# Kernel tuning notes

Measured on AMD Instinct MI355X. Metric: run time of the kernel, lower is better.

The kernel has to match this reference:

```python
import jax, jax.numpy as jnp
import numpy as np

B, N, E, H, D = 8, 1024, 512, 8, 64  # batch, tokens, embed, heads, dim_head


def setup_inputs() -> dict:
    key = jax.random.key(0)
    ks = jax.random.split(key, 12)
    f = lambda k, s: jax.random.normal(k, s, dtype=jnp.float32)
    return {
        "x": f(ks[0], (B, N, E)),
        "r_t": f(ks[1], (B, N, E)),
        "r_c": f(ks[2], (B, N, E)),
        "bias_time_e": f(ks[3], (H, D)) * 0.02,
        "bias_time_r": f(ks[4], (H, D)) * 0.02,
        "bias_channel_r": f(ks[5], (H, D)) * 0.02,
        "bias_channel_e": f(ks[6], (H, D)) * 0.02,
        "w_qkv": f(ks[7], (E, 3 * H * D)) * 0.02,   # to_qkv (no bias)
        "w_kr_t": f(ks[8], (E, H * D)) * 0.02,      # k_r_time_net (no bias)
        "w_kr_c": f(ks[9], (E, H * D)) * 0.02,      # k_r_channel_net (no bias)
        "w_out": f(ks[10], (H * D, E)) * 0.02,      # to_out Linear
        "b_out": f(ks[11], (E,)) * 0.02,
    }


def _rel_shift(x):
    # x: [i, j, b, h] -- TransformerXL relative shift along j
    i, j, b, h = x.shape
    zp = jnp.zeros((i, 1, b, h), x.dtype)
    xp = jnp.concatenate([zp, x], axis=1).reshape(j + 1, i, b, h)
    return xp[1:].reshape(i, j, b, h)


def reference(x, r_t, r_c, bias_time_e, bias_time_r, bias_channel_r, bias_channel_e,
              w_qkv, w_kr_t, w_kr_c, w_out, b_out):
    b, n, _ = x.shape
    to_nbhd = lambda t: t.reshape(b, n, H, D).transpose(1, 0, 2, 3)  # [n,b,h,d]
    q, k, v = jnp.split(x @ w_qkv, 3, axis=-1)
    q, k, v = to_nbhd(q), to_nbhd(k), to_nbhd(v)
    qb = q + bias_time_e  # broadcast [h,d] over [n,b,h,d]
    wr_t = to_nbhd(r_t @ w_kr_t)
    wr_c = to_nbhd(r_c @ w_kr_c)
    AC = jnp.einsum('ibhd,jbhd->ijbh', qb, k)
    BD_t = _rel_shift(jnp.einsum('ibhd,jbhd->ijbh', qb, wr_t))
    BD_c = _rel_shift(jnp.einsum('ibhd,jbhd->ijbh', qb, wr_c))
    dots = AC + (BD_t + BD_c) * 0.5
    # Faithful to torch: nn.Softmax(dim=-1) on [i,j,b,h] normalizes over HEADS.
    attn = jax.nn.softmax(dots, axis=-1)
    out = jnp.einsum('ijbh,jbhd->ibhd', attn, v)
    out = out.transpose(1, 0, 2, 3).reshape(b, n, H * D) @ w_out + b_out
    return out, attn.transpose(2, 3, 0, 1)  # ([b,n,E], [b,h,q,k])
```

## Files before the change

### kernel.cpp

```cpp
#include <hip/hip_runtime.h>
#include <hip/hip_fp16.h>


typedef _Float16 f16;
typedef f16 f16x4 __attribute__((ext_vector_type(4)));
typedef f16 f16x8 __attribute__((ext_vector_type(8)));
typedef float f32x4 __attribute__((ext_vector_type(4)));

#define MFMA16(a,b,c) __builtin_amdgcn_mfma_f32_16x16x32_f16((a),(b),(c),0,0,0)

static __device__ __forceinline__ size_t qpidx(int bh, int q, int d) {
  return ((((size_t)bh * 64 + (q >> 4)) * 2 + (d >> 5)) * 64 +
          ((q & 15) + (((d >> 3) & 3) << 4))) * 8 + (d & 7);
}
static __device__ __forceinline__ size_t vpidx(int bh, int d, int j) {
  return ((((size_t)bh * 4 + (d >> 4)) * 32 + (j >> 5)) * 64 +
          ((d & 15) + (((j >> 3) & 3) << 4))) * 8 + (j & 7);
}

__global__ __launch_bounds__(256) void kprep(
    const float* __restrict__ x, const float* __restrict__ rt, const float* __restrict__ rc,
    const float* __restrict__ wqkv, const float* __restrict__ wkrt, const float* __restrict__ wkrc,
    f16* __restrict__ X16, f16* __restrict__ A2, f16* __restrict__ WQ, f16* __restrict__ W2)
{
  const int t = threadIdx.x, gx = blockIdx.x, mode = blockIdx.y;
  if (mode <= 2) {
    const size_t id = (size_t)gx * 256 + t;
    const float* src = (mode == 0) ? x : (mode == 1) ? rt : rc;
    float4 v0 = *(const float4*)&src[id * 8];
    float4 v1 = *(const float4*)&src[id * 8 + 4];
    f16x8 o = {(f16)v0.x, (f16)v0.y, (f16)v0.z, (f16)v0.w,
               (f16)v1.x, (f16)v1.y, (f16)v1.z, (f16)v1.w};
    if (mode == 0) *(f16x8*)&X16[id * 8] = o;
    else {
      const int mrow = (int)(id >> 6), cc = (int)(id & 63);
      *(f16x8*)&A2[(size_t)mrow * 1024 + (mode == 2 ? 512 : 0) + cc * 8] = o;
    }
  } else if (mode == 3) {
    if (gx >= 384) return;
    const int c = gx & 63, n = (gx >> 6) * 256 + t;
    f16x8 o;
    #pragma unroll
    for (int e = 0; e < 8; ++e) o[e] = (f16)wqkv[(size_t)(c * 8 + e) * 1536 + n];
    *(f16x8*)&WQ[(size_t)n * 512 + c * 8] = o;
  } else {
    if (gx >= 128) return;
    const int c = gx & 63, n = (gx >> 6) * 256 + t;
    const float* src = (mode == 4) ? wkrt : wkrc;
    f16x8 o;
    #pragma unroll
    for (int e = 0; e < 8; ++e) o[e] = (f16)src[(size_t)(c * 8 + e) * 512 + n];
    *(f16x8*)&W2[(size_t)n * 1024 + (mode == 5 ? 512 : 0) + c * 8] = o;
  }
}

__global__ __launch_bounds__(256) void kproj(
    const f16* __restrict__ X16, const f16* __restrict__ A2,
    const f16* __restrict__ WQ, const f16* __restrict__ W2,
    const float* __restrict__ bias_te,
    f16* __restrict__ QP, f16* __restrict__ KP, f16* __restrict__ VP, f16* __restrict__ WP)
{
  __shared__ f16 As[128 * 64];
  __shared__ f16 Bs[128 * 64];
  const int t = threadIdx.x, l = t & 63, w = t >> 6;
  const int wr = w >> 1, wc = w & 1;
  const int m0 = blockIdx.x * 128;
  const int y = blockIdx.y;
  const int mode = y >> 2;
  const bool wrs = (mode == 3);
  const f16* Asrc = wrs ? A2 : X16;
  const int lda = wrs ? 1024 : 512;
  const int K = wrs ? 1024 : 512;
  const f16* Bsrc = wrs ? (W2 + (size_t)((y - 12) * 128) * 1024)
                        : (WQ + (size_t)(y * 128) * 512);
  const int ldb = wrs ? 1024 : 512;

  f32x4 acc[4][4] = {};
  for (int k0 = 0; k0 < K; k0 += 64) {
    __syncthreads();
    #pragma unroll
    for (int rep = 0; rep < 4; ++rep) {
      const int idx = rep * 256 + t;
      const int row = idx >> 3, kb = idx & 7;
      const int slot = (kb ^ (row & 7)) << 3;
      f16x8 va = *(const f16x8*)&Asrc[(size_t)(m0 + row) * lda + k0 + kb * 8];
      *(f16x8*)&As[row * 64 + slot] = va;
      f16x8 vb = *(const f16x8*)&Bsrc[(size_t)row * ldb + k0 + kb * 8];
      *(f16x8*)&Bs[row * 64 + slot] = vb;
    }
    __syncthreads();
    #pragma unroll
    for (int kc = 0; kc < 2; ++kc) {
      f16x8 af[4], bf[4];
      const int kb = kc * 4 + (l >> 4);
      #pragma unroll
      for (int mb = 0; mb < 4; ++mb) {
        const int r = wr * 64 + mb * 16 + (l & 15);
        af[mb] = *(const f16x8*)&As[r * 64 + ((kb ^ (r & 7)) << 3)];
      }
      #pragma unroll
      for (int nb = 0; nb < 4; ++nb) {
        const int r = wc * 64 + nb * 16 + (l & 15);
        bf[nb] = *(const f16x8*)&Bs[r * 64 + ((kb ^ (r & 7)) << 3)];
      }
      #pragma unroll
      for (int mb = 0; mb < 4; ++mb)
      #pragma unroll
      for (int nb = 0; nb < 4; ++nb)
        acc[mb][nb] = MFMA16(af[mb], bf[nb], acc[mb][nb]);
    }
  }
  #pragma unroll
  for (int mb = 0; mb < 4; ++mb)
  #pragma unroll
  for (int nb = 0; nb < 4; ++nb) {
    const int loc = wc * 64 + nb * 16 + (l & 15);
    const int c = (y & 3) * 128 + loc;
    const int hh = c >> 6, d = c & 63;
    const float badd = (mode == 0) ? bias_te[c] : 0.f;
    f32x4 a = acc[mb][nb];
    #pragma unroll
    for (int r = 0; r < 4; ++r) {
      const int m = m0 + wr * 64 + mb * 16 + (l >> 4) * 4 + r;
      const int bb = m >> 10, tn = m & 1023;
      const int bh = bb * 8 + hh;
      const float v = a[r] + badd;
      if (mode == 0)      QP[qpidx(bh, tn, d)] = (f16)v;
      else if (mode == 1) KP[qpidx(bh, tn, d)] = (f16)v;
      else if (mode == 2) VP[vpidx(bh, d, tn)] = (f16)v;
      else                WP[qpidx(bh, tn, d)] = (f16)v;
    }
  }
}

__global__ __launch_bounds__(512) void kdots(
    const f16* __restrict__ QP, const f16* __restrict__ KP,
    const f16* __restrict__ WP, float* __restrict__ attn_out)
{
  __shared__ f16 sd[8][32][72];
  const int t = threadIdx.x, l = t & 63, h = t >> 6;
  const int k0 = blockIdx.x * 64;
  const int q0 = blockIdx.y * 32;
  const int b = blockIdx.z;
  const int bh = b * 8 + h;
  const f16x8* QP8 = (const f16x8*)QP;
  const f16x8* KP8 = (const f16x8*)KP;
  const f16x8* WP8 = (const f16x8*)WP;
  f16x8 aq[3][2];
  #pragma unroll
  for (int mb = 0; mb < 3; ++mb)
  #pragma unroll
  for (int kc = 0; kc < 2; ++kc)
    aq[mb][kc] = QP8[((size_t)(bh * 64 + (q0 >> 4) + mb) * 2 + kc) * 64 + l];
  {
    f16* sdf = (f16*)sd;
    for (int i = t; i < 2304; i += 512) *(f16x8*)&sdf[(size_t)i * 8] = f16x8{};
  }
  __syncthreads();
  const int u0 = k0 - q0;
  const int qrow = (l >> 4) * 4;
  auto rawblock = [&](int jb) {
    f32x4 racc[3] = {};
    #pragma unroll
    for (int kc = 0; kc < 2; ++kc) {
      f16x8 bf = WP8[((size_t)(bh * 64 + jb) * 2 + kc) * 64 + l];
      #pragma unroll
      for (int mb = 0; mb < 3; ++mb)
        racc[mb] = MFMA16(aq[mb][kc], bf, racc[mb]);
    }
    const int jglob = jb * 16 + (l & 15);
    #pragma unroll
    for (int mb = 0; mb < 3; ++mb)
    #pragma unroll
    for (int r = 0; r < 4; ++r) {
      const int qloc = mb * 16 + qrow + r;
      const int a = q0 + qloc;
      const f16 v = (f16)(0.5f * racc[mb][r]);
      if (qloc < 32) {
        const int kA = a + jglob - 1023;
        if (kA >= k0 && kA < k0 + 64) sd[h][qloc][kA - k0] = v;
      }
      if (qloc >= 1 && qloc <= 32) {
        const int kB = a + jglob + 1;
        if (kB >= k0 && kB < k0 + 64) sd[h][qloc - 1][kB - k0] = v;
      }
    }
  };
  {
    const int blo_e = u0 - 33, bhi_e = (u0 + 61 > 1023) ? 1023 : u0 + 61;
    if (bhi_e >= 0) {
      const int blo = (blo_e < 0 ? 0 : blo_e) >> 4, bhi = bhi_e >> 4;
      for (int jb = blo; jb <= bhi; ++jb) rawblock(jb);
    }
    if (u0 <= 31) {
      const int alo_e = 992 + u0, ahi_e = (1086 + u0 > 1023) ? 1023 : 1086 + u0;
      const int alo = (alo_e < 0 ? 0 : alo_e) >> 4, ahi = ahi_e >> 4;
      for (int jb = alo; jb <= ahi; ++jb) rawblock(jb);
    }
  }
  __syncthreads();
  f32x4 acc[2][4] = {};
  #pragma unroll
  for (int kc = 0; kc < 2; ++kc) {
    #pragma unroll
    for (int nb = 0; nb < 4; ++nb) {
      f16x8 bf = KP8[((size_t)(bh * 64 + (k0 >> 4) + nb) * 2 + kc) * 64 + l];
      #pragma unroll
      for (int mb = 0; mb < 2; ++mb)
        acc[mb][nb] = MFMA16(aq[mb][kc], bf, acc[mb][nb]);
    }
  }
  #pragma unroll
  for (int mb = 0; mb < 2; ++mb)
  #pragma unroll
  for (int nb = 0; nb < 4; ++nb)
  #pragma unroll
  for (int r = 0; r < 4; ++r) {
    const int qloc = mb * 16 + qrow + r, kloc = nb * 16 + (l & 15);
    sd[h][qloc][kloc] = (f16)((float)sd[h][qloc][kloc] + acc[mb][nb][r]);
  }
  __syncthreads();
  {
    const int o = t * 4, q = o >> 6, k = o & 63;
    float dv[8][4];
    #pragma unroll
    for (int hh = 0; hh < 8; ++hh) {
      f16x4 v = *(const f16x4*)&sd[hh][q][k];
      dv[hh][0] = (float)v[0]; dv[hh][1] = (float)v[1];
      dv[hh][2] = (float)v[2]; dv[hh][3] = (float)v[3];
    }
    #pragma unroll
    for (int e = 0; e < 4; ++e) {
      float m = dv[0][e];
      #pragma unroll
      for (int hh = 1; hh < 8; ++hh) m = fmaxf(m, dv[hh][e]);
      float ssum = 0.f;
      #pragma unroll
      for (int hh = 0; hh < 8; ++hh) { float a = __expf(dv[hh][e] - m); dv[hh][e] = a; ssum += a; }
      float rinv = 1.f / ssum;
      #pragma unroll
      for (int hh = 0; hh < 8; ++hh) dv[hh][e] *= rinv;
    }
    const size_t qg = q0 + q;
    #pragma unroll
    for (int hh = 0; hh < 8; ++hh)
      *(float4*)&attn_out[((size_t)(b * 8 + hh) * 1024 + qg) * 1024 + k0 + k] =
          float4{dv[hh][0], dv[hh][1], dv[hh][2], dv[hh][3]};
  }
}

__global__ __launch_bounds__(256) void kpv(
    const float* __restrict__ attn, const f16* __restrict__ VP, f16* __restrict__ OUT1)
{
  __shared__ f16 at[128][72];
  const int t = threadIdx.x, l = t & 63, w = t >> 6;
  const int q0 = blockIdx.x * 128;
  const int bh = blockIdx.y;
  const int b = bh >> 3, h = bh & 7;
  const size_t abase = (size_t)bh * 1024 * 1024;
  const f16x8* VP8 = (const f16x8*)VP;
  f32x4 acc[2][4] = {};
  for (int j0 = 0; j0 < 1024; j0 += 64) {
    __syncthreads();
    #pragma unroll
    for (int rep = 0; rep < 8; ++rep) {
      int idx = rep * 1024 + t * 4;
      int q = idx >> 6, j = idx & 63;
      float4 v = *(const float4*)&attn[abase + (size_t)(q0 + q) * 1024 + j0 + j];
      *(f16x4*)&at[q][j] = f16x4{(f16)v.x, (f16)v.y, (f16)v.z, (f16)v.w};
    }
    __syncthreads();
    #pragma unroll
    for (int kc = 0; kc < 2; ++kc) {
      f16x8 pa[2];
      #pragma unroll
      for (int mb = 0; mb < 2; ++mb) {
        int row = w * 32 + mb * 16 + (l & 15);
        int jj = kc * 32 + (l >> 4) * 8;
        pa[mb] = *(const f16x8*)&at[row][jj];
      }
      #pragma unroll
      for (int nb = 0; nb < 4; ++nb) {
        f16x8 vb = VP8[(((size_t)bh * 4 + nb) * 32 + (j0 >> 5) + kc) * 64 + l];
        #pragma unroll
        for (int mb = 0; mb < 2; ++mb)
          acc[mb][nb] = MFMA16(pa[mb], vb, acc[mb][nb]);
      }
    }
  }
  #pragma unroll
  for (int mb = 0; mb < 2; ++mb)
  #pragma unroll
  for (int nb = 0; nb < 4; ++nb)
  #pragma unroll
  for (int r = 0; r < 4; ++r) {
    const int qg = q0 + w * 32 + mb * 16 + (l >> 4) * 4 + r;
    const int dd = nb * 16 + (l & 15);
    OUT1[((size_t)b * 1024 + qg) * 512 + h * 64 + dd] = (f16)acc[mb][nb][r];
  }
}

__global__ __launch_bounds__(256) void kout(
    const f16* __restrict__ OUT1, const float* __restrict__ w_out,
    const float* __restrict__ b_out, float* __restrict__ out)
{
  __shared__ f16 a_s[128][36];
  __shared__ f16 b_s[64][36];
  const int t = threadIdx.x, l = t & 63, w = t >> 6;
  const int m0 = blockIdx.x * 128;
  const int c0 = blockIdx.y * 64;
  f32x4 acc[2][4] = {};
  for (int k0 = 0; k0 < 512; k0 += 32) {
    __syncthreads();
    #pragma unroll
    for (int rep = 0; rep < 2; ++rep) {
      int idx = rep * 2048 + t * 8;
      int r = idx >> 5, c = idx & 31;
      f16x8 v = *(const f16x8*)&OUT1[(size_t)(m0 + r) * 512 + k0 + c];
      *(f16x4*)&a_s[r][c]     = f16x4{v[0], v[1], v[2], v[3]};
      *(f16x4*)&a_s[r][c + 4] = f16x4{v[4], v[5], v[6], v[7]};
    }
    #pragma unroll
    for (int rep = 0; rep < 2; ++rep) {
      int idx = rep * 1024 + t * 4;
      int kr = idx >> 6, c = idx & 63;
      float4 v = *(const float4*)&w_out[(size_t)(k0 + kr) * 512 + c0 + c];
      b_s[c + 0][kr] = (f16)v.x; b_s[c + 1][kr] = (f16)v.y;
      b_s[c + 2][kr] = (f16)v.z; b_s[c + 3][kr] = (f16)v.w;
    }
    __syncthreads();
    const int kc = (l >> 4) * 8;
    f16x8 af[2];
    #pragma unroll
    for (int mb = 0; mb < 2; ++mb) {
      int r = w * 32 + mb * 16 + (l & 15);
      af[mb] = __builtin_shufflevector(*(const f16x4*)&a_s[r][kc], *(const f16x4*)&a_s[r][kc + 4],
                                       0, 1, 2, 3, 4, 5, 6, 7);
    }
    #pragma unroll
    for (int nb = 0; nb < 4; ++nb) {
      int cc = nb * 16 + (l & 15);
      f16x8 bf = __builtin_shufflevector(*(const f16x4*)&b_s[cc][kc], *(const f16x4*)&b_s[cc][kc + 4],
                                         0, 1, 2, 3, 4, 5, 6, 7);
      #pragma unroll
      for (int mb = 0; mb < 2; ++mb)
        acc[mb][nb] = MFMA16(af[mb], bf, acc[mb][nb]);
    }
  }
  #pragma unroll
  for (int mb = 0; mb < 2; ++mb)
  #pragma unroll
  for (int nb = 0; nb < 4; ++nb) {
    const int cg = c0 + nb * 16 + (l & 15);
    const float bb = b_out[cg];
    #pragma unroll
    for (int r = 0; r < 4; ++r) {
      const int m = m0 + w * 32 + mb * 16 + (l >> 4) * 4 + r;
      out[(size_t)m * 512 + cg] = acc[mb][nb][r] + bb;
    }
  }
}

extern "C" void kernel_launch(void* const* d_in, const int* in_sizes, int n_in,
                              void* d_out, int out_size, void* d_ws, size_t ws_size,
                              hipStream_t stream) {
  const float* x       = (const float*)d_in[0];
  const float* rt      = (const float*)d_in[1];
  const float* rc      = (const float*)d_in[2];
  const float* bias_te = (const float*)d_in[3];
  const float* w_qkv   = (const float*)d_in[7];
  const float* w_kr_t  = (const float*)d_in[8];
  const float* w_kr_c  = (const float*)d_in[9];
  const float* w_out   = (const float*)d_in[10];
  const float* b_out   = (const float*)d_in[11];
  float* out = (float*)d_out;
  float* attn_out = out + (size_t)8 * 1024 * 512;

  const size_t oX16 = 0;
  const size_t oA2  = oX16 + 4194304;
  const size_t oWQ  = oA2  + 8388608;
  const size_t oW2  = oWQ  + 786432;
  const size_t oQP  = oW2  + 524288;
  const size_t oKP  = oQP  + 4194304;
  const size_t oVP  = oKP  + 4194304;
  const size_t oWP  = oVP  + 4194304;
  const size_t oO1  = oWP  + 4194304;
  const size_t NEEDED = (oO1 + 4194304) * 2;
  if (ws_size < NEEDED) return;
  f16* ws = (f16*)d_ws;
  f16 *X16 = ws + oX16, *A2 = ws + oA2, *WQ = ws + oWQ, *W2 = ws + oW2;
  f16 *QP = ws + oQP, *KP = ws + oKP, *VP = ws + oVP, *WP = ws + oWP;
  f16 *OUT1 = ws + oO1;

  kprep<<<dim3(2048, 6), 256, 0, stream>>>(x, rt, rc, w_qkv, w_kr_t, w_kr_c,
                                           X16, A2, WQ, W2);
  kproj<<<dim3(64, 16), 256, 0, stream>>>(X16, A2, WQ, W2, bias_te, QP, KP, VP, WP);
  kdots<<<dim3(16, 32, 8), 512, 0, stream>>>(QP, KP, WP, attn_out);
  kpv<<<dim3(8, 64), 256, 0, stream>>>(attn_out, VP, OUT1);
  kout<<<dim3(64, 8), 256, 0, stream>>>(OUT1, w_out, b_out, out);
}
```

Before: 257.1 us.

## Fuse attention-times-V into dots kernel with split-K partial outputs

The separate kpv kernel, which re-read the full fp32 attention matrix from global memory, is removed. kdots now loops over four key tiles per block, keeps the softmaxed probabilities in shared memory as f16 and multiplies them by V directly, accumulating into registers. Each of the four key groups writes an fp32 partial output, and kout sums the four partials while loading its A operand. This avoids re-reading the large attention tensor, at the cost of extra fp32 partial-output traffic, a 4x smaller kdots grid and added syncs per tile.

```diff
diff --git a/kernel.cpp b/kernel.cpp
--- a/kernel.cpp
+++ b/kernel.cpp
@@ -133,141 +133,130 @@
   }
 }
 
-__global__ __launch_bounds__(512) void kdots(
+__global__ __launch_bounds__(512, 4) void kdots(
     const f16* __restrict__ QP, const f16* __restrict__ KP,
-    const f16* __restrict__ WP, float* __restrict__ attn_out)
+    const f16* __restrict__ WP, const f16* __restrict__ VP,
+    float* __restrict__ attn_out, float* __restrict__ OUTP)
 {
   __shared__ f16 sd[8][32][72];
   const int t = threadIdx.x, l = t & 63, h = t >> 6;
-  const int k0 = blockIdx.x * 64;
+  const int kg = blockIdx.x;
   const int q0 = blockIdx.y * 32;
   const int b = blockIdx.z;
   const int bh = b * 8 + h;
   const f16x8* QP8 = (const f16x8*)QP;
   const f16x8* KP8 = (const f16x8*)KP;
   const f16x8* WP8 = (const f16x8*)WP;
+  const f16x8* VP8 = (const f16x8*)VP;
+  const int qrow = (l >> 4) * 4;
   f16x8 aq[3][2];
   #pragma unroll
   for (int mb = 0; mb < 3; ++mb)
   #pragma unroll
   for (int kc = 0; kc < 2; ++kc)
     aq[mb][kc] = QP8[((size_t)(bh * 64 + (q0 >> 4) + mb) * 2 + kc) * 64 + l];
-  {
-    f16* sdf = (f16*)sd;
-    for (int i = t; i < 2304; i += 512) *(f16x8*)&sdf[(size_t)i * 8] = f16x8{};
-  }
-  __syncthreads();
-  const int u0 = k0 - q0;
-  const int qrow = (l >> 4) * 4;
-  auto rawblock = [&](int jb) {
-    f32x4 racc[3] = {};
-    #pragma unroll
-    for (int kc = 0; kc < 2; ++kc) {
-      f16x8 bf = WP8[((size_t)(bh * 64 + jb) * 2 + kc) * 64 + l];
+
+  f32x4 oacc[2][4] = {};
+
+  for (int kti = 0; kti < 4; ++kti) {
+    const int k0 = (kg * 4 + kti) * 64;
+    {
+      f16* sdf = (f16*)sd;
+      for (int i = t; i < 2304; i += 512) *(f16x8*)&sdf[(size_t)i * 8] = f16x8{};
+    }
+    __syncthreads();
+    const int u0 = k0 - q0;
+    auto rawblock = [&](int jb) {
+      f32x4 racc[3] = {};
+      #pragma unroll
+      for (int kc = 0; kc < 2; ++kc) {
+        f16x8 bf = WP8[((size_t)(bh * 64 + jb) * 2 + kc) * 64 + l];
+        #pragma unroll
+        for (int mb = 0; mb < 3; ++mb)
+          racc[mb] = MFMA16(aq[mb][kc], bf, racc[mb]);
+      }
+      const int jglob = jb * 16 + (l & 15);
       #pragma unroll
       for (int mb = 0; mb < 3; ++mb)
-        racc[mb] = MFMA16(aq[mb][kc], bf, racc[mb]);
-    }
-    const int jglob = jb * 16 + (l & 15);
-    #pragma unroll
-    for (int mb = 0; mb < 3; ++mb)
-    #pragma unroll
-    for (int r = 0; r < 4; ++r) {
-      const int qloc = mb * 16 + qrow + r;
-      const int a = q0 + qloc;
-      const f16 v = (f16)(0.5f * racc[mb][r]);
-      if (qloc < 32) {
-        const int kA = a + jglob - 1023;
-        if (kA >= k0 && kA < k0 + 64) sd[h][qloc][kA - k0] = v;
-      }
-      if (qloc >= 1 && qloc <= 32) {
-        const int kB = a + jglob + 1;
-        if (kB >= k0 && kB < k0 + 64) sd[h][qloc - 1][kB - k0] = v;
-      }
-    }
-  };
-  {
-    const int blo_e = u0 - 33, bhi_e = (u0 + 61 > 1023) ? 1023 : u0 + 61;
-    if (bhi_e >= 0) {
-      const int blo = (blo_e < 0 ? 0 : blo_e) >> 4, bhi = bhi_e >> 4;
-      for (int jb = blo; jb <= bhi; ++jb) rawblock(jb);
-    }
-    if (u0 <= 31) {
-      const int alo_e = 992 + u0, ahi_e = (1086 + u0 > 1023) ? 1023 : 1086 + u0;
-      const int alo = (alo_e < 0 ? 0 : alo_e) >> 4, ahi = ahi_e >> 4;
-      for (int jb = alo; jb <= ahi; ++jb) rawblock(jb);
-    }
-  }
-  __syncthreads();
-  f32x4 acc[2][4] = {};
-  #pragma unroll
-  for (int kc = 0; kc < 2; ++kc) {
-    #pragma unroll
-    for (int nb = 0; nb < 4; ++nb) {
-      f16x8 bf = KP8[((size_t)(bh * 64 + (k0 >> 4) + nb) * 2 + kc) * 64 + l];
+      #pragma unroll
+      for (int r = 0; r < 4; ++r) {
+        const int qloc = mb * 16 + qrow + r;
+        const int a = q0 + qloc;
+        const f16 v = (f16)(0.5f * racc[mb][r]);
+        if (qloc < 32) {
+          const int kA = a + jglob - 1023;
+          if (kA >= k0 && kA < k0 + 64) sd[h][qloc][kA - k0] = v;
+        }
+        if (qloc >= 1 && qloc <= 32) {
+          const int kB = a + jglob + 1;
+          if (kB >= k0 && kB < k0 + 64) sd[h][qloc - 1][kB - k0] = v;
+        }
+      }
+    };
+    {
+      const int blo_e = u0 - 33, bhi_e = (u0 + 61 > 1023) ? 1023 : u0 + 61;
+      if (bhi_e >= 0) {
+        const int blo = (blo_e < 0 ? 0 : blo_e) >> 4, bhi = bhi_e >> 4;
+        for (int jb = blo; jb <= bhi; ++jb) rawblock(jb);
+      }
+      if (u0 <= 31) {
+        const int alo_e = 992 + u0, ahi_e = (1086 + u0 > 1023) ? 1023 : 1086 + u0;
+        const int alo = (alo_e < 0 ? 0 : alo_e) >> 4, ahi = ahi_e >> 4;
+        for (int jb = alo; jb <= ahi; ++jb) rawblock(jb);
+      }
+    }
+    {
+      f32x4 acc[2][4] = {};
+      #pragma unroll
+      for (int kc = 0; kc < 2; ++kc) {
+        #pragma unroll
+        for (int nb = 0; nb < 4; ++nb) {
+          f16x8 bf = KP8[((size_t)(bh * 64 + (k0 >> 4) + nb) * 2 + kc) * 64 + l];
+          #pragma unroll
+          for (int mb = 0; mb < 2; ++mb)
+            acc[mb][nb] = MFMA16(aq[mb][kc], bf, acc[mb][nb]);
+        }
+      }
       #pragma unroll
       for (int mb = 0; mb < 2; ++mb)
-        acc[mb][nb] = MFMA16(aq[mb][kc], bf, acc[mb][nb]);
-    }
-  }
-  #pragma unroll
-  for (int mb = 0; mb < 2; ++mb)
-  #pragma unroll
-  for (int nb = 0; nb < 4; ++nb)
-  #pragma unroll
-  for (int r = 0; r < 4; ++r) {
-    const int qloc = mb * 16 + qrow + r, kloc = nb * 16 + (l & 15);
-    sd[h][qloc][kloc] = (f16)((float)sd[h][qloc][kloc] + acc[mb][nb][r]);
-  }
-  __syncthreads();
-  {
-    const int o = t * 4, q = o >> 6, k = o & 63;
-    float dv[8][4];
-    #pragma unroll
-    for (int hh = 0; hh < 8; ++hh) {
-      f16x4 v = *(const f16x4*)&sd[hh][q][k];
-      dv[hh][0] = (float)v[0]; dv[hh][1] = (float)v[1];
-      dv[hh][2] = (float)v[2]; dv[hh][3] = (float)v[3];
-    }
-    #pragma unroll
-    for (int e = 0; e < 4; ++e) {
-      float m = dv[0][e];
-      #pragma unroll
-      for (int hh = 1; hh < 8; ++hh) m = fmaxf(m, dv[hh][e]);
-      float ssum = 0.f;
-      #pragma unroll
-      for (int hh = 0; hh < 8; ++hh) { float a = __expf(dv[hh][e] - m); dv[hh][e] = a; ssum += a; }
-      float rinv = 1.f / ssum;
-      #pragma unroll
-      for (int hh = 0; hh < 8; ++hh) dv[hh][e] *= rinv;
-    }
-    const size_t qg = q0 + q;
-    #pragma unroll
-    for (int hh = 0; hh < 8; ++hh)
-      *(float4*)&attn_out[((size_t)(b * 8 + hh) * 1024 + qg) * 1024 + k0 + k] =
-          float4{dv[hh][0], dv[hh][1], dv[hh][2], dv[hh][3]};
-  }
-}
-
-__global__ __launch_bounds__(256) void kpv(
-    const float* __restrict__ attn, const f16* __restrict__ VP, f16* __restrict__ OUT1)
-{
-  __shared__ f16 at[128][72];
-  const int t = threadIdx.x, l = t & 63, w = t >> 6;
-  const int q0 = blockIdx.x * 128;
-  const int bh = blockIdx.y;
-  const int b = bh >> 3, h = bh & 7;
-  const size_t abase = (size_t)bh * 1024 * 1024;
-  const f16x8* VP8 = (const f16x8*)VP;
-  f32x4 acc[2][4] = {};
-  for (int j0 = 0; j0 < 1024; j0 += 64) {
-    __syncthreads();
-    #pragma unroll
-    for (int rep = 0; rep < 8; ++rep) {
-      int idx = rep * 1024 + t * 4;
-      int q = idx >> 6, j = idx & 63;
-      float4 v = *(const float4*)&attn[abase + (size_t)(q0 + q) * 1024 + j0 + j];
-      *(f16x4*)&at[q][j] = f16x4{(f16)v.x, (f16)v.y, (f16)v.z, (f16)v.w};
+      #pragma unroll
+      for (int nb = 0; nb < 4; ++nb)
+      #pragma unroll
+      for (int r = 0; r < 4; ++r) {
+        const int qloc = mb * 16 + qrow + r, kloc = nb * 16 + (l & 15);
+        sd[h][qloc][kloc] = (f16)((float)sd[h][qloc][kloc] + acc[mb][nb][r]);
+      }
+    }
+    __syncthreads();
+    {
+      const int o = t * 4, q = o >> 6, k = o & 63;
+      float dv[8][4];
+      #pragma unroll
+      for (int hh = 0; hh < 8; ++hh) {
+        f16x4 v = *(const f16x4*)&sd[hh][q][k];
+        dv[hh][0] = (float)v[0]; dv[hh][1] = (float)v[1];
+        dv[hh][2] = (float)v[2]; dv[hh][3] = (float)v[3];
+      }
+      #pragma unroll
+      for (int e = 0; e < 4; ++e) {
+        float m = dv[0][e];
+        #pragma unroll
+        for (int hh = 1; hh < 8; ++hh) m = fmaxf(m, dv[hh][e]);
+        float ssum = 0.f;
+        #pragma unroll
+        for (int hh = 0; hh < 8; ++hh) { float a = __expf(dv[hh][e] - m); dv[hh][e] = a; ssum += a; }
+        float rinv = 1.f / ssum;
+        #pragma unroll
+        for (int hh = 0; hh < 8; ++hh) dv[hh][e] *= rinv;
+      }
+      const size_t qg = q0 + q;
+      #pragma unroll
+      for (int hh = 0; hh < 8; ++hh) {
+        *(float4*)&attn_out[((size_t)(b * 8 + hh) * 1024 + qg) * 1024 + k0 + k] =
+            float4{dv[hh][0], dv[hh][1], dv[hh][2], dv[hh][3]};
+        *(f16x4*)&sd[hh][q][k] =
+            f16x4{(f16)dv[hh][0], (f16)dv[hh][1], (f16)dv[hh][2], (f16)dv[hh][3]};
+      }
     }
     __syncthreads();
     #pragma unroll
@@ -275,33 +264,35 @@
       f16x8 pa[2];
       #pragma unroll
       for (int mb = 0; mb < 2; ++mb) {
-        int row = w * 32 + mb * 16 + (l & 15);
-        int jj = kc * 32 + (l >> 4) * 8;
-        pa[mb] = *(const f16x8*)&at[row][jj];
+        const int qq = mb * 16 + (l & 15);
+        const int jj = kc * 32 + (l >> 4) * 8;
+        pa[mb] = *(const f16x8*)&sd[h][qq][jj];
       }
       #pragma unroll
       for (int nb = 0; nb < 4; ++nb) {
-        f16x8 vb = VP8[(((size_t)bh * 4 + nb) * 32 + (j0 >> 5) + kc) * 64 + l];
+        f16x8 vb = VP8[(((size_t)bh * 4 + nb) * 32 + (k0 >> 5) + kc) * 64 + l];
         #pragma unroll
         for (int mb = 0; mb < 2; ++mb)
-          acc[mb][nb] = MFMA16(pa[mb], vb, acc[mb][nb]);
-      }
-    }
-  }
+          oacc[mb][nb] = MFMA16(pa[mb], vb, oacc[mb][nb]);
+      }
+    }
+    __syncthreads();
+  }
+  float* op = OUTP + ((size_t)kg * 8192 + (size_t)b * 1024) * 512;
   #pragma unroll
   for (int mb = 0; mb < 2; ++mb)
   #pragma unroll
   for (int nb = 0; nb < 4; ++nb)
   #pragma unroll
   for (int r = 0; r < 4; ++r) {
-    const int qg = q0 + w * 32 + mb * 16 + (l >> 4) * 4 + r;
+    const int qg = q0 + mb * 16 + qrow + r;
     const int dd = nb * 16 + (l & 15);
-    OUT1[((size_t)b * 1024 + qg) * 512 + h * 64 + dd] = (f16)acc[mb][nb][r];
+    op[(size_t)qg * 512 + h * 64 + dd] = oacc[mb][nb][r];
   }
 }
 
 __global__ __launch_bounds__(256) void kout(
-    const f16* __restrict__ OUT1, const float* __restrict__ w_out,
+    const float* __restrict__ OUTP, const float* __restrict__ w_out,
     const float* __restrict__ b_out, float* __restrict__ out)
 {
   __shared__ f16 a_s[128][36];
@@ -313,12 +304,18 @@
   for (int k0 = 0; k0 < 512; k0 += 32) {
     __syncthreads();
     #pragma unroll
-    for (int rep = 0; rep < 2; ++rep) {
-      int idx = rep * 2048 + t * 8;
-      int r = idx >> 5, c = idx & 31;
-      f16x8 v = *(const f16x8*)&OUT1[(size_t)(m0 + r) * 512 + k0 + c];
-      *(f16x4*)&a_s[r][c]     = f16x4{v[0], v[1], v[2], v[3]};
-      *(f16x4*)&a_s[r][c + 4] = f16x4{v[4], v[5], v[6], v[7]};
+    for (int rep = 0; rep < 4; ++rep) {
+      const int s = rep * 256 + t;
+      const int r = s >> 3, c = (s & 7) * 4;
+      const size_t off = (size_t)(m0 + r) * 512 + k0 + c;
+      float4 v0 = *(const float4*)&OUTP[off];
+      float4 v1 = *(const float4*)&OUTP[off + 4194304];
+      float4 v2 = *(const float4*)&OUTP[off + 8388608];
+      float4 v3 = *(const float4*)&OUTP[off + 12582912];
+      *(f16x4*)&a_s[r][c] = f16x4{(f16)(v0.x + v1.x + v2.x + v3.x),
+                                  (f16)(v0.y + v1.y + v2.y + v3.y),
+                                  (f16)(v0.z + v1.z + v2.z + v3.z),
+                                  (f16)(v0.w + v1.w + v2.w + v3.w)};
     }
     #pragma unroll
     for (int rep = 0; rep < 2; ++rep) {
@@ -384,18 +381,17 @@
   const size_t oKP  = oQP  + 4194304;
   const size_t oVP  = oKP  + 4194304;
   const size_t oWP  = oVP  + 4194304;
-  const size_t oO1  = oWP  + 4194304;
-  const size_t NEEDED = (oO1 + 4194304) * 2;
+  const size_t oOP  = oWP  + 4194304;
+  const size_t NEEDED = oOP * 2 + (size_t)4 * 8192 * 512 * 4;
   if (ws_size < NEEDED) return;
   f16* ws = (f16*)d_ws;
   f16 *X16 = ws + oX16, *A2 = ws + oA2, *WQ = ws + oWQ, *W2 = ws + oW2;
   f16 *QP = ws + oQP, *KP = ws + oKP, *VP = ws + oVP, *WP = ws + oWP;
-  f16 *OUT1 = ws + oO1;
+  float* OUTP = (float*)(ws + oOP);
 
   kprep<<<dim3(2048, 6), 256, 0, stream>>>(x, rt, rc, w_qkv, w_kr_t, w_kr_c,
                                            X16, A2, WQ, W2);
   kproj<<<dim3(64, 16), 256, 0, stream>>>(X16, A2, WQ, W2, bias_te, QP, KP, VP, WP);
-  kdots<<<dim3(16, 32, 8), 512, 0, stream>>>(QP, KP, WP, attn_out);
-  kpv<<<dim3(8, 64), 256, 0, stream>>>(attn_out, VP, OUT1);
-  kout<<<dim3(64, 8), 256, 0, stream>>>(OUT1, w_out, b_out, out);
-}
+  kdots<<<dim3(4, 32, 8), 512, 0, stream>>>(QP, KP, WP, VP, attn_out, OUTP);
+  kout<<<dim3(64, 8), 256, 0, stream>>>(OUTP, w_out, b_out, out);
+}
```

Result: slower. 267.9 us (+4.2%).
